# Kernel optimization log

Hardware: AMD Instinct MI355X
Metric: run time of the kernel (lower is better)

The kernel has to match this reference:

```python
import jax, jax.numpy as jnp
import numpy as np

N_NODES = 100000
DIM_IN = 128
DIM_H = 64
LATENT = 64
N_EDGES = 1200000


def setup_inputs() -> dict:
    key = jax.random.key(0)
    ks = jax.random.split(key, 8)
    x = jax.random.normal(ks[0], (N_NODES, DIM_IN), dtype=jnp.float32)
    edge_index = jax.random.randint(ks[1], (2, N_EDGES), 0, N_NODES, dtype=jnp.int32)
    batch = jnp.zeros((N_NODES,), dtype=jnp.int32)
    s_in = 1.0 / np.sqrt(DIM_IN)
    s_h = 1.0 / np.sqrt(DIM_H)
    gcn_w = jax.random.uniform(ks[2], (DIM_IN, DIM_H), jnp.float32, -s_in, s_in)
    gcn_b = jnp.zeros((DIM_H,), dtype=jnp.float32)
    w1 = jax.random.uniform(ks[3], (DIM_H, LATENT), jnp.float32, -s_h, s_h)
    b1 = jax.random.uniform(ks[4], (LATENT,), jnp.float32, -s_h, s_h)
    s_l = 1.0 / np.sqrt(LATENT)
    w3 = jax.random.uniform(ks[5], (LATENT, LATENT), jnp.float32, -s_l, s_l)
    b3 = jax.random.uniform(ks[6], (LATENT,), jnp.float32, -s_l, s_l)
    return {"x": x, "edge_index": edge_index, "batch": batch,
            "gcn_w": gcn_w, "gcn_b": gcn_b, "w1": w1, "b1": b1, "w3": w3, "b3": b3}


def _gcn_conv(x, edge_index, W, b):
    n = x.shape[0]
    loop = jnp.arange(n, dtype=edge_index.dtype)
    src = jnp.concatenate([edge_index[0], loop])
    dst = jnp.concatenate([edge_index[1], loop])
    deg = jax.ops.segment_sum(jnp.ones_like(dst, dtype=x.dtype), dst, num_segments=n)
    dinv = jnp.where(deg > 0, jax.lax.rsqrt(deg), 0.0)
    norm = dinv[src] * dinv[dst]                      # [E+N]
    h = x @ W                                          # [N, dim_h]
    msg = h[src] * norm[:, None]                       # gather + scale
    out = jax.ops.segment_sum(msg, dst, num_segments=n)  # scatter-add
    return out + b


def reference(x, edge_index, batch, gcn_w, gcn_b, w1, b1, w3, b3):
    g1 = _gcn_conv(x, edge_index, gcn_w, gcn_b)
    l1 = g1 @ w1 + b1
    l3 = l1 @ w3 + b3
    # mu/sigma/z/kl in the original are side effects not returned; output is l3
    return l3
```

## Files before the change

kernel.cpp:

```cpp
#include <hip/hip_runtime.h>
#include <hip/hip_bf16.h>

#define N_NODES 100000
#define N_EDGES 1200000
#define NBK 256
#define NPB 391
#define NSUB 8
#define CAPS 2048
#define CAPB 5376
#define EPB 4096
#define BIN_BLKS 293
#define XW_BLKS 1280
#define FUSED_GRID (BIN_BLKS + XW_BLKS)
#define GB 2048

typedef __attribute__((ext_vector_type(8))) short bf16x8;
typedef __attribute__((ext_vector_type(4))) float f32x4;

__global__ __launch_bounds__(256) void k_w(const float* __restrict__ gcn_w,
                                           const float* __restrict__ gcn_b,
                                           const float* __restrict__ w1,
                                           const float* __restrict__ b1,
                                           const float* __restrict__ w3,
                                           const float* __restrict__ b3,
                                           short* __restrict__ WcB,
                                           float* __restrict__ bc,
                                           int* __restrict__ bcnt8) {
    __shared__ float tmp[4096];
    __shared__ float tb[64];
    const int b = blockIdx.x, t = threadIdx.x;
    if (b == 31)
        for (int i = t; i < NBK * NSUB; i += 256) bcnt8[i] = 0;
    if (b == 0 && t < 64) {
        float s = b1[t];
        for (int k = 0; k < 64; ++k) s = fmaf(gcn_b[k], w1[k * 64 + t], s);
        tb[t] = s;
    }
    for (int i = t; i < 4096; i += 256) {
        const int r = i >> 6, c = i & 63;
        float a = 0.f;
#pragma unroll 8
        for (int k = 0; k < 64; ++k) a = fmaf(w1[r * 64 + k], w3[k * 64 + c], a);
        tmp[i] = a;
    }
    __syncthreads();
    const int i = b * 256 + t;
    const int r = i >> 6, c = i & 63;
    float a = 0.f;
#pragma unroll 8
    for (int k = 0; k < 64; ++k) a = fmaf(gcn_w[r * 64 + k], tmp[k * 64 + c], a);
    const int kt = r >> 5, kr = r & 31, g = kr >> 3, e = kr & 7;
    const int ct = c & 3, cl = c >> 2, lane = g * 16 + cl;
    WcB[(((kt * 4 + ct) * 64) + lane) * 8 + e] =
        __builtin_bit_cast(short, __float2bfloat16(a));
    if (b == 0 && t < 64) {
        float s = b3[t];
        for (int k = 0; k < 64; ++k) s = fmaf(tb[k], w3[k * 64 + t], s);
        bc[t] = s;
    }
}

__global__ __launch_bounds__(256) void k_fused(const int* __restrict__ ei,
                                               int* __restrict__ bcnt8,
                                               int* __restrict__ binned,
                                               const float* __restrict__ x,
                                               const short* __restrict__ WcB,
                                               unsigned char* __restrict__ hsq,
                                               float* __restrict__ hscale) {
    const int b = blockIdx.x;
    if (b < BIN_BLKS) {
        __shared__ int hist[NBK], base[NBK], cur[NBK];
        const int t = threadIdx.x;
        const int e0 = b * EPB;
        const int nrem = min(EPB, N_EDGES - e0);
        unsigned xcd;
        asm volatile("s_getreg_b32 %0, hwreg(HW_REG_XCC_ID)" : "=s"(xcd));
        xcd &= 7;
        for (int i = t; i < NBK; i += 256) hist[i] = 0;

        const int tb = t * 16;
        const int cnt = max(0, min(16, nrem - tb));
        int s_r[16], d_r[16];
        if (tb + 15 < nrem) {
#pragma unroll
            for (int u = 0; u < 4; ++u) {
                const int4 s4 = *(const int4*)(ei + e0 + tb + u * 4);
                const int4 d4 = *(const int4*)(ei + N_EDGES + e0 + tb + u * 4);
                s_r[u * 4 + 0] = s4.x; s_r[u * 4 + 1] = s4.y;
                s_r[u * 4 + 2] = s4.z; s_r[u * 4 + 3] = s4.w;
                d_r[u * 4 + 0] = d4.x; d_r[u * 4 + 1] = d4.y;
                d_r[u * 4 + 2] = d4.z; d_r[u * 4 + 3] = d4.w;
            }
        } else {
#pragma unroll
            for (int k = 0; k < 16; ++k) {
                const int e = tb + k;
                s_r[k] = (e < nrem) ? ei[e0 + e] : 0;
                d_r[k] = (e < nrem) ? ei[N_EDGES + e0 + e] : 0;
            }
        }
        int bk_r[16], dl_r[16];
#pragma unroll
        for (int k = 0; k < 16; ++k) {
            const int d = d_r[k];
            const int bk = d / NPB;
            bk_r[k] = bk;
            dl_r[k] = d - bk * NPB;
        }
        __syncthreads();
#pragma unroll
        for (int k = 0; k < 16; ++k)
            if (k < cnt) atomicAdd(&hist[bk_r[k]], 1);
        __syncthreads();
        for (int i = t; i < NBK; i += 256) {
            const int h = hist[i];
            base[i] = h ? atomicAdd(&bcnt8[i * NSUB + xcd], h) : 0;
            cur[i] = 0;
        }
        __syncthreads();
#pragma unroll
        for (int k = 0; k < 16; ++k) {
            if (k < cnt) {
                const int bk = bk_r[k];
                const int p = base[bk] + atomicAdd(&cur[bk], 1);
                if (p < CAPS)
                    binned[((size_t)(bk * NSUB + xcd)) * CAPS + p] =
                        s_r[k] | (dl_r[k] << 17);
            }
        }
    } else {
        const int t = threadIdx.x, w = t >> 6, lane = t & 63;
        const int cl = lane & 15, g = lane >> 4;
        bf16x8 bfrag[16];
#pragma unroll
        for (int f = 0; f < 16; ++f) bfrag[f] = ((const bf16x8*)WcB)[f * 64 + lane];

        const int ntiles = N_NODES / 16;
        const int nw = XW_BLKS * 4;
        for (int tile = (b - BIN_BLKS) * 4 + w; tile < ntiles; tile += nw) {
            const int node0 = tile * 16;
            const float* xrow = x + (size_t)(node0 + cl) * 128 + g * 8;
            f32x4 xa[4][2];
#pragma unroll
            for (int kt = 0; kt < 4; ++kt) {
                xa[kt][0] = *(const f32x4*)(xrow + kt * 32);
                xa[kt][1] = *(const f32x4*)(xrow + kt * 32 + 4);
            }
            f32x4 acc[4];
#pragma unroll
            for (int ct = 0; ct < 4; ++ct) acc[ct] = (f32x4){0.f, 0.f, 0.f, 0.f};
#pragma unroll
            for (int kt = 0; kt < 4; ++kt) {
                bf16x8 af;
#pragma unroll
                for (int j = 0; j < 4; ++j) {
                    af[j]     = __builtin_bit_cast(short, __float2bfloat16(xa[kt][0][j]));
                    af[j + 4] = __builtin_bit_cast(short, __float2bfloat16(xa[kt][1][j]));
                }
#pragma unroll
                for (int ct = 0; ct < 4; ++ct)
                    acc[ct] = __builtin_amdgcn_mfma_f32_16x16x32_bf16(
                        af, bfrag[kt * 4 + ct], acc[ct], 0, 0, 0);
            }
            float mx[4];
#pragma unroll
            for (int j = 0; j < 4; ++j) {
                mx[j] = fmaxf(fmaxf(fabsf(acc[0][j]), fabsf(acc[1][j])),
                              fmaxf(fabsf(acc[2][j]), fabsf(acc[3][j])));
            }
#pragma unroll
            for (int m = 1; m < 16; m <<= 1)
#pragma unroll
                for (int j = 0; j < 4; ++j)
                    mx[j] = fmaxf(mx[j], __shfl_xor(mx[j], m));
#pragma unroll
            for (int j = 0; j < 4; ++j) {
                const float sc = fmaxf(mx[j], 1e-20f) * (1.f / 127.f);
                const float inv = 127.f / fmaxf(mx[j], 1e-20f);
                unsigned int pk = 0;
#pragma unroll
                for (int ct = 0; ct < 4; ++ct) {
                    const int v = (int)rintf(acc[ct][j] * inv);
                    pk |= ((unsigned int)(v & 0xFF)) << (8 * ct);
                }
                *(unsigned int*)(hsq + (size_t)(node0 + g * 4 + j) * 64 + cl * 4) = pk;
                if (cl == j) hscale[node0 + g * 4 + j] = sc;
            }
        }
    }
}

__global__ __launch_bounds__(512) void k_csr(const int* __restrict__ bcnt8,
                                             const int* __restrict__ binned,
                                             const float* __restrict__ hscale,
                                             int* __restrict__ csr,
                                             int* __restrict__ rowptr,
                                             int* __restrict__ degA,
                                             float* __restrict__ dinv,
                                             float* __restrict__ csca) {
    __shared__ int stage[CAPB];
    __shared__ int sdeg[NPB], sloc[NPB], scur[NPB];
    __shared__ int soff[NSUB + 1];
    const int b = blockIdx.x, t = threadIdx.x;
    if (t == 0) {
        int o = 0;
#pragma unroll
        for (int k = 0; k < NSUB; ++k) {
            soff[k] = o;
            const int c = min(bcnt8[b * NSUB + k], CAPS);
            o = min(o + c, CAPB);
        }
        soff[NSUB] = o;
    }
    for (int i = t; i < NPB; i += 512) { sdeg[i] = 0; scur[i] = 0; }
    __syncthreads();
    const int m = soff[NSUB];
#pragma unroll
    for (int k = 0; k < NSUB; ++k) {
        const int n = soff[k + 1] - soff[k];
        for (int j = t; j < n; j += 512)
            stage[soff[k] + j] = binned[((size_t)(b * NSUB + k)) * CAPS + j];
    }
    __syncthreads();
    for (int j = t; j < m; j += 512) atomicAdd(&sdeg[stage[j] >> 17], 1);
    __syncthreads();
    if (t < 64) {
        int run = 0;
#pragma unroll
        for (int c0 = 0; c0 < NPB; c0 += 64) {
            const int idx = c0 + t;
            const int v = (idx < NPB) ? sdeg[idx] : 0;
            int inc = v;
#pragma unroll
            for (int o = 1; o < 64; o <<= 1) {
                const int u = __shfl_up(inc, o);
                if (t >= o) inc += u;
            }
            if (idx < NPB) sloc[idx] = run + inc - v;
            run += __shfl(inc, 63);
        }
    }
    __syncthreads();
    for (int i = t; i < NPB; i += 512) {
        const int node = b * NPB + i;
        if (node < N_NODES) {
            const int v = sdeg[i];
            const float dv = rsqrtf((float)(v + 1));
            rowptr[node] = b * CAPB + sloc[i];
            degA[node] = v;
            dinv[node] = dv;
            csca[node] = dv * hscale[node];
        }
    }
    for (int j = t; j < m; j += 512) {
        const int pk = stage[j];
        const int dl = pk >> 17;
        const int p = atomicAdd(&scur[dl], 1);
        csr[b * CAPB + sloc[dl] + p] = pk & 0x1FFFF;
    }
}

__global__ __launch_bounds__(256) void k_gather(const int* __restrict__ rowptr,
                                                const int* __restrict__ degA,
                                                const int* __restrict__ csr,
                                                const unsigned char* __restrict__ hsq,
                                                const float* __restrict__ csca,
                                                const float* __restrict__ dinv,
                                                const float* __restrict__ bc,
                                                float* __restrict__ out) {
    const int t = threadIdx.x, wv = t >> 6, lane = t & 63;
    const int cl = lane & 15, g = lane >> 4, cc = cl * 4;
    const int NW = GB * 4;
    int n = blockIdx.x * 4 + wv;
    const float4 bc4 = *(const float4*)(bc + cc);

    int deg0 = degA[n], base0 = rowptr[n];
    float dvn0 = dinv[n], csn0 = csca[n];
    unsigned qs0 = *(const unsigned*)(hsq + (size_t)n * 64 + cc);
    int s0 = 0; float c0 = 0.f;
    {
        const int r = min(deg0, 64);
        if (lane < r) { s0 = csr[base0 + lane]; c0 = csca[s0]; }
    }
    int n1 = n + NW;
    int deg1 = 0, base1 = 0; float dvn1 = 0.f, csn1 = 0.f; unsigned qs1 = 0;
    if (n1 < N_NODES) {
        deg1 = degA[n1]; base1 = rowptr[n1];
        dvn1 = dinv[n1]; csn1 = csca[n1];
        qs1 = *(const unsigned*)(hsq + (size_t)n1 * 64 + cc);
    }

    for (;;) {
        const int r1 = min(deg1, 64);
        int s1 = 0;
        if (n1 < N_NODES && lane < r1) s1 = csr[base1 + lane];
        const int n2 = n1 + NW;
        int deg2 = 0, base2 = 0; float dvn2 = 0.f, csn2 = 0.f; unsigned qs2 = 0;
        if (n2 < N_NODES) {
            deg2 = degA[n2]; base2 = rowptr[n2];
            dvn2 = dinv[n2]; csn2 = csca[n2];
            qs2 = *(const unsigned*)(hsq + (size_t)n2 * 64 + cc);
        }
        f32x4 acc = (f32x4){0.f, 0.f, 0.f, 0.f};
        const int r0 = min(deg0, 64);
        for (int i0 = 0; i0 < r0; i0 += 16) {
#pragma unroll
            for (int u = 0; u < 4; ++u) {
                const int jj = i0 + u * 4 + g;
                const int sj = __shfl(s0, jj);
                const float cj = __shfl(c0, jj);
                if (jj < r0) {
                    const unsigned q = *(const unsigned*)(hsq + (size_t)sj * 64 + cc);
                    acc[0] = fmaf((float)(int)(signed char)(q & 0xFFu), cj, acc[0]);
                    acc[1] = fmaf((float)(int)(signed char)((q >> 8) & 0xFFu), cj, acc[1]);
                    acc[2] = fmaf((float)(int)(signed char)((q >> 16) & 0xFFu), cj, acc[2]);
                    acc[3] = fmaf((float)(int)(signed char)(q >> 24), cj, acc[3]);
                }
            }
        }
        for (int j0 = 64; j0 < deg0; j0 += 64) {
            const int rem = min(deg0 - j0, 64);
            int sl = 0; float clv = 0.f;
            if (lane < rem) { sl = csr[base0 + j0 + lane]; clv = csca[sl]; }
            for (int i0 = 0; i0 < rem; i0 += 16) {
#pragma unroll
                for (int u = 0; u < 4; ++u) {
                    const int jj = i0 + u * 4 + g;
                    const int sj = __shfl(sl, jj);
                    const float cj = __shfl(clv, jj);
                    if (jj < rem) {
                        const unsigned q = *(const unsigned*)(hsq + (size_t)sj * 64 + cc);
                        acc[0] = fmaf((float)(int)(signed char)(q & 0xFFu), cj, acc[0]);
                        acc[1] = fmaf((float)(int)(signed char)((q >> 8) & 0xFFu), cj, acc[1]);
                        acc[2] = fmaf((float)(int)(signed char)((q >> 16) & 0xFFu), cj, acc[2]);
                        acc[3] = fmaf((float)(int)(signed char)(q >> 24), cj, acc[3]);
                    }
                }
            }
        }
#pragma unroll
        for (int k = 0; k < 4; ++k) {
            acc[k] += __shfl_xor(acc[k], 16);
            acc[k] += __shfl_xor(acc[k], 32);
        }
        float4 res;
        res.x = fmaf(fmaf((float)(int)(signed char)(qs0 & 0xFFu), csn0, acc[0]), dvn0, bc4.x);
        res.y = fmaf(fmaf((float)(int)(signed char)((qs0 >> 8) & 0xFFu), csn0, acc[1]), dvn0, bc4.y);
        res.z = fmaf(fmaf((float)(int)(signed char)((qs0 >> 16) & 0xFFu), csn0, acc[2]), dvn0, bc4.z);
        res.w = fmaf(fmaf((float)(int)(signed char)(qs0 >> 24), csn0, acc[3]), dvn0, bc4.w);
        if (g == 0) *(float4*)(out + (size_t)n * 64 + cc) = res;

        if (n1 >= N_NODES) break;
        float c1 = 0.f;
        if (lane < r1) c1 = csca[s1];
        n = n1; deg0 = deg1; base0 = base1; dvn0 = dvn1; csn0 = csn1;
        qs0 = qs1; s0 = s1; c0 = c1;
        n1 = n2; deg1 = deg2; base1 = base2; dvn1 = dvn2; csn1 = csn2; qs1 = qs2;
    }
}

extern "C" void kernel_launch(void* const* d_in, const int* in_sizes, int n_in,
                              void* d_out, int out_size, void* d_ws, size_t ws_size,
                              hipStream_t stream) {
    const float* x     = (const float*)d_in[0];
    const int*   ei    = (const int*)d_in[1];
    const float* gcn_w = (const float*)d_in[3];
    const float* gcn_b = (const float*)d_in[4];
    const float* w1    = (const float*)d_in[5];
    const float* b1    = (const float*)d_in[6];
    const float* w3    = (const float*)d_in[7];
    const float* b3    = (const float*)d_in[8];
    float* out = (float*)d_out;

    char* ws = (char*)d_ws;
    int*           bcnt8  = (int*)(ws);
    short*         WcB    = (short*)(ws + 8192);
    float*         bc     = (float*)(ws + 24576);
    float*         dinv   = (float*)(ws + 24832);
    int*           rowptr = (int*)(ws + 424832);
    int*           degA   = (int*)(ws + 824832);
    float*         hscale = (float*)(ws + 1224832);
    float*         csca   = (float*)(ws + 1624832);
    unsigned char* hsq    = (unsigned char*)(ws + 2024832);
    int*           binned = (int*)(ws + 8424832);
    int*           csr    = (int*)(ws + 25202048);

    k_w<<<32, 256, 0, stream>>>(gcn_w, gcn_b, w1, b1, w3, b3, WcB, bc, bcnt8);
    k_fused<<<FUSED_GRID, 256, 0, stream>>>(ei, bcnt8, binned, x, WcB, hsq, hscale);
    k_csr<<<NBK, 512, 0, stream>>>(bcnt8, binned, hscale, csr, rowptr, degA, dinv, csca);
    k_gather<<<GB, 256, 0, stream>>>(rowptr, degA, csr, hsq, csca, dinv, bc, out);
}
```

Before: 100.6 us.

## Regroup kernels: fuse weight prep with binning, CSR build with XW GEMM

Reorganises the pipeline into a memset plus three kernels. Weight folding now runs alongside edge binning in one launch, and the CSR build runs alongside the x·W quantized GEMM in another. This removes one dependency boundary and lets independent phases overlap. The precomputed csca array is dropped: k_gather now computes dinv*hscale on the fly, which adds an extra gathered load per neighbour. The GEMM side now uses 512-thread blocks with 8 waves, which changes occupancy, and shared memory for the CSR stage is reserved even in the GEMM blocks.

```diff
diff --git a/kernel.cpp b/kernel.cpp
--- a/kernel.cpp
+++ b/kernel.cpp
@@ -10,82 +10,75 @@
 #define CAPB 5376
 #define EPB 4096
 #define BIN_BLKS 293
-#define XW_BLKS 1280
-#define FUSED_GRID (BIN_BLKS + XW_BLKS)
+#define W_BLKS 32
+#define BW_GRID (W_BLKS + BIN_BLKS)
+#define XW_BLKS2 640
+#define XC_GRID (NBK + XW_BLKS2)
 #define GB 2048
 
 typedef __attribute__((ext_vector_type(8))) short bf16x8;
 typedef __attribute__((ext_vector_type(4))) float f32x4;
 
-__global__ __launch_bounds__(256) void k_w(const float* __restrict__ gcn_w,
-                                           const float* __restrict__ gcn_b,
-                                           const float* __restrict__ w1,
-                                           const float* __restrict__ b1,
-                                           const float* __restrict__ w3,
-                                           const float* __restrict__ b3,
-                                           short* __restrict__ WcB,
-                                           float* __restrict__ bc,
-                                           int* __restrict__ bcnt8) {
-    __shared__ float tmp[4096];
-    __shared__ float tb[64];
+__global__ __launch_bounds__(256) void k_bw(const float* __restrict__ gcn_w,
+                                            const float* __restrict__ gcn_b,
+                                            const float* __restrict__ w1,
+                                            const float* __restrict__ b1,
+                                            const float* __restrict__ w3,
+                                            const float* __restrict__ b3,
+                                            short* __restrict__ WcB,
+                                            float* __restrict__ bc,
+                                            const int* __restrict__ ei,
+                                            int* __restrict__ bcnt8,
+                                            int* __restrict__ binned) {
     const int b = blockIdx.x, t = threadIdx.x;
-    if (b == 31)
-        for (int i = t; i < NBK * NSUB; i += 256) bcnt8[i] = 0;
-    if (b == 0 && t < 64) {
-        float s = b1[t];
-        for (int k = 0; k < 64; ++k) s = fmaf(gcn_b[k], w1[k * 64 + t], s);
-        tb[t] = s;
-    }
-    for (int i = t; i < 4096; i += 256) {
+    if (b < W_BLKS) {
+        __shared__ float tmp[4096];
+        __shared__ float tb[64];
+        if (b == 0 && t < 64) {
+            float s = b1[t];
+            for (int k = 0; k < 64; ++k) s = fmaf(gcn_b[k], w1[k * 64 + t], s);
+            tb[t] = s;
+        }
+        for (int i = t; i < 4096; i += 256) {
+            const int r = i >> 6, c = i & 63;
+            float a = 0.f;
+#pragma unroll 8
+            for (int k = 0; k < 64; ++k) a = fmaf(w1[r * 64 + k], w3[k * 64 + c], a);
+            tmp[i] = a;
+        }
+        __syncthreads();
+        const int i = b * 256 + t;
         const int r = i >> 6, c = i & 63;
         float a = 0.f;
 #pragma unroll 8
-        for (int k = 0; k < 64; ++k) a = fmaf(w1[r * 64 + k], w3[k * 64 + c], a);
-        tmp[i] = a;
-    }
-    __syncthreads();
-    const int i = b * 256 + t;
-    const int r = i >> 6, c = i & 63;
-    float a = 0.f;
-#pragma unroll 8
-    for (int k = 0; k < 64; ++k) a = fmaf(gcn_w[r * 64 + k], tmp[k * 64 + c], a);
-    const int kt = r >> 5, kr = r & 31, g = kr >> 3, e = kr & 7;
-    const int ct = c & 3, cl = c >> 2, lane = g * 16 + cl;
-    WcB[(((kt * 4 + ct) * 64) + lane) * 8 + e] =
-        __builtin_bit_cast(short, __float2bfloat16(a));
-    if (b == 0 && t < 64) {
-        float s = b3[t];
-        for (int k = 0; k < 64; ++k) s = fmaf(tb[k], w3[k * 64 + t], s);
-        bc[t] = s;
-    }
-}
-
-__global__ __launch_bounds__(256) void k_fused(const int* __restrict__ ei,
-                                               int* __restrict__ bcnt8,
-                                               int* __restrict__ binned,
-                                               const float* __restrict__ x,
-                                               const short* __restrict__ WcB,
-                                               unsigned char* __restrict__ hsq,
-                                               float* __restrict__ hscale) {
-    const int b = blockIdx.x;
-    if (b < BIN_BLKS) {
+        for (int k = 0; k < 64; ++k) a = fmaf(gcn_w[r * 64 + k], tmp[k * 64 + c], a);
+        const int kt = r >> 5, kr = r & 31, g = kr >> 3, e = kr & 7;
+        const int ct = c & 3, cl = c >> 2, lane = g * 16 + cl;
+        WcB[(((kt * 4 + ct) * 64) + lane) * 8 + e] =
+            __builtin_bit_cast(short, __float2bfloat16(a));
+        if (b == 0 && t < 64) {
+            float s = b3[t];
+            for (int k = 0; k < 64; ++k) s = fmaf(tb[k], w3[k * 64 + t], s);
+            bc[t] = s;
+        }
+    } else {
         __shared__ int hist[NBK], base[NBK], cur[NBK];
-        const int t = threadIdx.x;
-        const int e0 = b * EPB;
+        const int bb = b - W_BLKS;
+        const int e0 = bb * EPB;
         const int nrem = min(EPB, N_EDGES - e0);
         unsigned xcd;
         asm volatile("s_getreg_b32 %0, hwreg(HW_REG_XCC_ID)" : "=s"(xcd));
         xcd &= 7;
         for (int i = t; i < NBK; i += 256) hist[i] = 0;
 
-        const int tb = t * 16;
-        const int cnt = max(0, min(16, nrem - tb));
+        const int tb2 = t * 16;
+        const int cnt = max(0, min(16, nrem - tb2));
         int s_r[16], d_r[16];
-        if (tb + 15 < nrem) {
+        if (tb2 + 15 < nrem) {
 #pragma unroll
             for (int u = 0; u < 4; ++u) {
-                const int4 s4 = *(const int4*)(ei + e0 + tb + u * 4);
-                const int4 d4 = *(const int4*)(ei + N_EDGES + e0 + tb + u * 4);
+                const int4 s4 = *(const int4*)(ei + e0 + tb2 + u * 4);
+                const int4 d4 = *(const int4*)(ei + N_EDGES + e0 + tb2 + u * 4);
                 s_r[u * 4 + 0] = s4.x; s_r[u * 4 + 1] = s4.y;
                 s_r[u * 4 + 2] = s4.z; s_r[u * 4 + 3] = s4.w;
                 d_r[u * 4 + 0] = d4.x; d_r[u * 4 + 1] = d4.y;
@@ -94,7 +87,7 @@
         } else {
 #pragma unroll
             for (int k = 0; k < 16; ++k) {
-                const int e = tb + k;
+                const int e = tb2 + k;
                 s_r[k] = (e < nrem) ? ei[e0 + e] : 0;
                 d_r[k] = (e < nrem) ? ei[N_EDGES + e0 + e] : 0;
             }
@@ -128,16 +121,89 @@
                         s_r[k] | (dl_r[k] << 17);
             }
         }
+    }
+}
+
+__global__ __launch_bounds__(512) void k_xc(const int* __restrict__ bcnt8,
+                                            const int* __restrict__ binned,
+                                            int* __restrict__ csr,
+                                            int* __restrict__ rowptr,
+                                            int* __restrict__ degA,
+                                            float* __restrict__ dinv,
+                                            const float* __restrict__ x,
+                                            const short* __restrict__ WcB,
+                                            unsigned char* __restrict__ hsq,
+                                            float* __restrict__ hscale) {
+    __shared__ int stage[CAPB];
+    __shared__ int sdeg[NPB], sloc[NPB], scur[NPB];
+    __shared__ int soff[NSUB + 1];
+    const int blk = blockIdx.x, t = threadIdx.x;
+    if (blk < NBK) {
+        const int b = blk;
+        if (t == 0) {
+            int o = 0;
+#pragma unroll
+            for (int k = 0; k < NSUB; ++k) {
+                soff[k] = o;
+                const int c = min(bcnt8[b * NSUB + k], CAPS);
+                o = min(o + c, CAPB);
+            }
+            soff[NSUB] = o;
+        }
+        for (int i = t; i < NPB; i += 512) { sdeg[i] = 0; scur[i] = 0; }
+        __syncthreads();
+        const int m = soff[NSUB];
+#pragma unroll
+        for (int k = 0; k < NSUB; ++k) {
+            const int n = soff[k + 1] - soff[k];
+            for (int j = t; j < n; j += 512)
+                stage[soff[k] + j] = binned[((size_t)(b * NSUB + k)) * CAPS + j];
+        }
+        __syncthreads();
+        for (int j = t; j < m; j += 512) atomicAdd(&sdeg[stage[j] >> 17], 1);
+        __syncthreads();
+        if (t < 64) {
+            int run = 0;
+#pragma unroll
+            for (int c0 = 0; c0 < NPB; c0 += 64) {
+                const int idx = c0 + t;
+                const int v = (idx < NPB) ? sdeg[idx] : 0;
+                int inc = v;
+#pragma unroll
+                for (int o = 1; o < 64; o <<= 1) {
+                    const int u = __shfl_up(inc, o);
+                    if (t >= o) inc += u;
+                }
+                if (idx < NPB) sloc[idx] = run + inc - v;
+                run += __shfl(inc, 63);
+            }
+        }
+        __syncthreads();
+        for (int i = t; i < NPB; i += 512) {
+            const int node = b * NPB + i;
+            if (node < N_NODES) {
+                const int v = sdeg[i];
+                rowptr[node] = b * CAPB + sloc[i];
+                degA[node] = v;
+                dinv[node] = rsqrtf((float)(v + 1));
+            }
+        }
+        for (int j = t; j < m; j += 512) {
+            const int pk = stage[j];
+            const int dl = pk >> 17;
+            const int p = atomicAdd(&scur[dl], 1);
+            csr[b * CAPB + sloc[dl] + p] = pk & 0x1FFFF;
+        }
     } else {
-        const int t = threadIdx.x, w = t >> 6, lane = t & 63;
+        const int w = t >> 6, lane = t & 63;
         const int cl = lane & 15, g = lane >> 4;
         bf16x8 bfrag[16];
 #pragma unroll
         for (int f = 0; f < 16; ++f) bfrag[f] = ((const bf16x8*)WcB)[f * 64 + lane];
 
         const int ntiles = N_NODES / 16;
-        const int nw = XW_BLKS * 4;
-        for (int tile = (b - BIN_BLKS) * 4 + w; tile < ntiles; tile += nw) {
+        const int nw = XW_BLKS2 * 8;
+        for (int tile = (blk - NBK) * 8 + w; tile < ntiles; tile += nw) {
             const int node0 = tile * 16;
             const float* xrow = x + (size_t)(node0 + cl) * 128 + g * 8;
             f32x4 xa[4][2];
@@ -190,81 +256,11 @@
     }
 }
 
-__global__ __launch_bounds__(512) void k_csr(const int* __restrict__ bcnt8,
-                                             const int* __restrict__ binned,
-                                             const float* __restrict__ hscale,
-                                             int* __restrict__ csr,
-                                             int* __restrict__ rowptr,
-                                             int* __restrict__ degA,
-                                             float* __restrict__ dinv,
-                                             float* __restrict__ csca) {
-    __shared__ int stage[CAPB];
-    __shared__ int sdeg[NPB], sloc[NPB], scur[NPB];
-    __shared__ int soff[NSUB + 1];
-    const int b = blockIdx.x, t = threadIdx.x;
-    if (t == 0) {
-        int o = 0;
-#pragma unroll
-        for (int k = 0; k < NSUB; ++k) {
-            soff[k] = o;
-            const int c = min(bcnt8[b * NSUB + k], CAPS);
-            o = min(o + c, CAPB);
-        }
-        soff[NSUB] = o;
-    }
-    for (int i = t; i < NPB; i += 512) { sdeg[i] = 0; scur[i] = 0; }
-    __syncthreads();
-    const int m = soff[NSUB];
-#pragma unroll
-    for (int k = 0; k < NSUB; ++k) {
-        const int n = soff[k + 1] - soff[k];
-        for (int j = t; j < n; j += 512)
-            stage[soff[k] + j] = binned[((size_t)(b * NSUB + k)) * CAPS + j];
-    }
-    __syncthreads();
-    for (int j = t; j < m; j += 512) atomicAdd(&sdeg[stage[j] >> 17], 1);
-    __syncthreads();
-    if (t < 64) {
-        int run = 0;
-#pragma unroll
-        for (int c0 = 0; c0 < NPB; c0 += 64) {
-            const int idx = c0 + t;
-            const int v = (idx < NPB) ? sdeg[idx] : 0;
-            int inc = v;
-#pragma unroll
-            for (int o = 1; o < 64; o <<= 1) {
-                const int u = __shfl_up(inc, o);
-                if (t >= o) inc += u;
-            }
-            if (idx < NPB) sloc[idx] = run + inc - v;
-            run += __shfl(inc, 63);
-        }
-    }
-    __syncthreads();
-    for (int i = t; i < NPB; i += 512) {
-        const int node = b * NPB + i;
-        if (node < N_NODES) {
-            const int v = sdeg[i];
-            const float dv = rsqrtf((float)(v + 1));
-            rowptr[node] = b * CAPB + sloc[i];
-            degA[node] = v;
-            dinv[node] = dv;
-            csca[node] = dv * hscale[node];
-        }
-    }
-    for (int j = t; j < m; j += 512) {
-        const int pk = stage[j];
-        const int dl = pk >> 17;
-        const int p = atomicAdd(&scur[dl], 1);
-        csr[b * CAPB + sloc[dl] + p] = pk & 0x1FFFF;
-    }
-}
-
 __global__ __launch_bounds__(256) void k_gather(const int* __restrict__ rowptr,
                                                 const int* __restrict__ degA,
                                                 const int* __restrict__ csr,
                                                 const unsigned char* __restrict__ hsq,
-                                                const float* __restrict__ csca,
+                                                const float* __restrict__ hscale,
                                                 const float* __restrict__ dinv,
                                                 const float* __restrict__ bc,
                                                 float* __restrict__ out) {
@@ -275,18 +271,18 @@
     const float4 bc4 = *(const float4*)(bc + cc);
 
     int deg0 = degA[n], base0 = rowptr[n];
-    float dvn0 = dinv[n], csn0 = csca[n];
+    float dvn0 = dinv[n], csn0 = dvn0 * hscale[n];
     unsigned qs0 = *(const unsigned*)(hsq + (size_t)n * 64 + cc);
     int s0 = 0; float c0 = 0.f;
     {
         const int r = min(deg0, 64);
-        if (lane < r) { s0 = csr[base0 + lane]; c0 = csca[s0]; }
+        if (lane < r) { s0 = csr[base0 + lane]; c0 = dinv[s0] * hscale[s0]; }
     }
     int n1 = n + NW;
     int deg1 = 0, base1 = 0; float dvn1 = 0.f, csn1 = 0.f; unsigned qs1 = 0;
     if (n1 < N_NODES) {
         deg1 = degA[n1]; base1 = rowptr[n1];
-        dvn1 = dinv[n1]; csn1 = csca[n1];
+        dvn1 = dinv[n1]; csn1 = dvn1 * hscale[n1];
         qs1 = *(const unsigned*)(hsq + (size_t)n1 * 64 + cc);
     }
 
@@ -298,7 +294,7 @@
         int deg2 = 0, base2 = 0; float dvn2 = 0.f, csn2 = 0.f; unsigned qs2 = 0;
         if (n2 < N_NODES) {
             deg2 = degA[n2]; base2 = rowptr[n2];
-            dvn2 = dinv[n2]; csn2 = csca[n2];
+            dvn2 = dinv[n2]; csn2 = dvn2 * hscale[n2];
             qs2 = *(const unsigned*)(hsq + (size_t)n2 * 64 + cc);
         }
         f32x4 acc = (f32x4){0.f, 0.f, 0.f, 0.f};
@@ -321,7 +317,10 @@
         for (int j0 = 64; j0 < deg0; j0 += 64) {
             const int rem = min(deg0 - j0, 64);
             int sl = 0; float clv = 0.f;
-            if (lane < rem) { sl = csr[base0 + j0 + lane]; clv = csca[sl]; }
+            if (lane < rem) {
+                sl = csr[base0 + j0 + lane];
+                clv = dinv[sl] * hscale[sl];
+            }
             for (int i0 = 0; i0 < rem; i0 += 16) {
 #pragma unroll
                 for (int u = 0; u < 4; ++u) {
@@ -352,7 +351,7 @@
 
         if (n1 >= N_NODES) break;
         float c1 = 0.f;
-        if (lane < r1) c1 = csca[s1];
+        if (lane < r1) c1 = dinv[s1] * hscale[s1];
         n = n1; deg0 = deg1; base0 = base1; dvn0 = dvn1; csn0 = csn1;
         qs0 = qs1; s0 = s1; c0 = c1;
         n1 = n2; deg1 = deg2; base1 = base2; dvn1 = dvn2; csn1 = csn2; qs1 = qs2;
@@ -380,13 +379,14 @@
     int*           rowptr = (int*)(ws + 424832);
     int*           degA   = (int*)(ws + 824832);
     float*         hscale = (float*)(ws + 1224832);
-    float*         csca   = (float*)(ws + 1624832);
-    unsigned char* hsq    = (unsigned char*)(ws + 2024832);
-    int*           binned = (int*)(ws + 8424832);
-    int*           csr    = (int*)(ws + 25202048);
-
-    k_w<<<32, 256, 0, stream>>>(gcn_w, gcn_b, w1, b1, w3, b3, WcB, bc, bcnt8);
-    k_fused<<<FUSED_GRID, 256, 0, stream>>>(ei, bcnt8, binned, x, WcB, hsq, hscale);
-    k_csr<<<NBK, 512, 0, stream>>>(bcnt8, binned, hscale, csr, rowptr, degA, dinv, csca);
-    k_gather<<<GB, 256, 0, stream>>>(rowptr, degA, csr, hsq, csca, dinv, bc, out);
+    unsigned char* hsq    = (unsigned char*)(ws + 1624832);
+    int*           binned = (int*)(ws + 8024832);
+    int*           csr    = (int*)(ws + 24802048);
+
+    hipMemsetAsync(bcnt8, 0, (size_t)NBK * NSUB * sizeof(int), stream);
+    k_bw<<<BW_GRID, 256, 0, stream>>>(gcn_w, gcn_b, w1, b1, w3, b3, WcB, bc,
+                                      ei, bcnt8, binned);
+    k_xc<<<XC_GRID, 512, 0, stream>>>(bcnt8, binned, csr, rowptr, degA, dinv,
+                                      x, WcB, hsq, hscale);
+    k_gather<<<GB, 256, 0, stream>>>(rowptr, degA, csr, hsq, hscale, dinv, bc, out);
 }
```

After: 100.6 us (median of 3 runs). About the same (+0.0%).
